# Optimization experiments

Measured on AMD Instinct MI355X. Metric: run time of the kernel, lower is better.

Reference implementation:

```python
import jax, jax.numpy as jnp
import numpy as np
from jax import lax

K = 31      # avg_pool kernel
PAD = 15    # padding (count_include_pad=True -> divide by K*K always)
LAMBDA1 = 1.0
LAMBDA2 = 1.0


def _box_mean(x):
    # 31x31 stride-1 avg pool with zero padding, divisor = K*K (torch default count_include_pad=True)
    s = lax.reduce_window(x, 0.0, lax.add, (1, 1, K, K), (1, 1, 1, 1),
                          [(0, 0), (0, 0), (PAD, PAD), (PAD, PAD)])
    return s / float(K * K)


def setup_inputs() -> dict:
    key = jax.random.key(0)
    k1, k2 = jax.random.split(key)
    pred = jax.random.normal(k1, (64, 1, 512, 512), dtype=jnp.float32)
    mask = jax.random.uniform(k2, (64, 1, 512, 512), dtype=jnp.float32)
    return {"pred": pred, "mask": mask}


def reference(pred, mask):
    weit = 1.0 + 5.0 * jnp.abs(_box_mean(mask) - mask)
    # bce_with_logits, numerically stable: max(x,0) - x*y + log1p(exp(-|x|))
    bce = jnp.maximum(pred, 0.0) - pred * mask + jnp.log1p(jnp.exp(-jnp.abs(pred)))
    # NOTE: original torch code passes reduce='none' (deprecated kwarg, truthy string),
    # which resolves to reduction='mean' -> wbce is a SCALAR; the (weit*.)/weit.sum
    # normalization then cancels exactly. We reproduce that behavior faithfully.
    wbce = jnp.mean(bce)  # scalar, broadcast over (B, C)
    p = jax.nn.sigmoid(pred)
    inter = jnp.sum(p * mask * weit, axis=(2, 3))       # [B, C]
    union = jnp.sum((p + mask) * weit, axis=(2, 3))     # [B, C]
    wiou = 1.0 - (inter + 1.0) / (union - inter + 1.0)  # [B, C]
    return jnp.mean(LAMBDA1 * wbce + LAMBDA2 * wiou)
```

## Files before the change

### kernel.cpp

```cpp
#include <hip/hip_runtime.h>
#include <math.h>

#define BATCH 64
#define HH 512
#define WW 512
#define PAD 15
#define NELEM ((size_t)BATCH * HH * WW)
#define INV_KK (1.0f / 961.0f)

#define TILE_H 32
#define BPI (HH / TILE_H)
#define NBLK (BATCH * BPI)

typedef float f4 __attribute__((ext_vector_type(4)));

__device__ __forceinline__ float wave_reduce(float v) {
    #pragma unroll
    for (int off = 32; off; off >>= 1) v += __shfl_down(v, off, 64);
    return v;
}

__global__ __launch_bounds__(256) void fused_kernel(const float* __restrict__ pred,
                                                    const float* __restrict__ mask,
                                                    double* __restrict__ partials) {
    __shared__ float vrow[4][WW];
    __shared__ float P[4][WW];
    __shared__ float red[3][4];

    const int blk  = blockIdx.x;
    const int b    = blk >> 4;
    const int tile = blk & (BPI - 1);
    const int h0   = tile * TILE_H;
    const int tid  = threadIdx.x;
    const int lane = tid & 63;
    const int wv   = tid >> 6;

    const float* mb = mask + (size_t)b * HH * WW;
    const float* pb = pred + (size_t)b * HH * WW;

    const int c0 = tid, c1 = tid + 256;
    float r0 = 0.f, r1 = 0.f;
    {
        int lo = h0 - PAD; if (lo < 0) lo = 0;
        for (int y = lo; y <= h0 + PAD; ++y) {
            r0 += mb[(size_t)y * WW + c0];
            r1 += mb[(size_t)y * WW + c1];
        }
    }

    float accb = 0.f, acci = 0.f, accu = 0.f;

    for (int it = 0; it < TILE_H / 4; ++it) {
        const int hbase = h0 + it * 4;

        #pragma unroll
        for (int j = 0; j < 4; ++j) {
            const int h = hbase + j;
            vrow[j][c0] = r0;
            vrow[j][c1] = r1;
            const int add = h + PAD + 1;
            const int sub = h - PAD;
            float a0 = 0.f, a1 = 0.f, s0 = 0.f, s1 = 0.f;
            if (add < HH) { a0 = mb[(size_t)add * WW + c0]; a1 = mb[(size_t)add * WW + c1]; }
            if (sub >= 0) { s0 = mb[(size_t)sub * WW + c0]; s1 = mb[(size_t)sub * WW + c1]; }
            r0 += a0 - s0;
            r1 += a1 - s1;
        }
        __syncthreads();

        const int h = hbase + wv;
        const size_t rbase = (size_t)h * WW;

        f4 va = *(const f4*)&vrow[wv][8 * lane];
        f4 vb = *(const f4*)&vrow[wv][8 * lane + 4];
        float p0 = va.x;
        float p1 = p0 + va.y;
        float p2 = p1 + va.z;
        float p3 = p2 + va.w;
        float p4 = p3 + vb.x;
        float p5 = p4 + vb.y;
        float p6 = p5 + vb.z;
        float p7 = p6 + vb.w;
        float lanesum = p7;
        float incl = lanesum;
        #pragma unroll
        for (int off = 1; off < 64; off <<= 1) {
            float n = __shfl_up(incl, off, 64);
            if (lane >= off) incl += n;
        }
        const float excl = incl - lanesum;
        f4 Pa, Pb;
        Pa.x = excl + p0; Pa.y = excl + p1; Pa.z = excl + p2; Pa.w = excl + p3;
        Pb.x = excl + p4; Pb.y = excl + p5; Pb.z = excl + p6; Pb.w = excl + p7;
        *(f4*)&P[wv][8 * lane]     = Pa;
        *(f4*)&P[wv][8 * lane + 4] = Pb;
        __syncthreads();

        #pragma unroll
        for (int k = 0; k < 8; ++k) {
            const int w = lane + 64 * k;
            int hiw = w + PAD; if (hiw > WW - 1) hiw = WW - 1;
            float s = P[wv][hiw];
            if (w >= PAD + 1) s -= P[wv][w - PAD - 1];

            const float m  = mb[rbase + w];
            const float pr = pb[rbase + w];

            const float weit = 1.0f + 5.0f * fabsf(s * INV_KK - m);
            const float e    = __expf(-fabsf(pr));
            const float bce  = fmaxf(pr, 0.f) - pr * m + __logf(1.0f + e);
            const float inv  = __builtin_amdgcn_rcpf(1.0f + e);
            const float p    = (pr >= 0.f) ? inv : e * inv;

            accb += bce;
            acci += p * m * weit;
            accu += (p + m) * weit;
        }
    }

    accb = wave_reduce(accb);
    acci = wave_reduce(acci);
    accu = wave_reduce(accu);
    if (lane == 0) { red[0][wv] = accb; red[1][wv] = acci; red[2][wv] = accu; }
    __syncthreads();
    if (tid == 0) {
        double bt = (double)red[0][0] + red[0][1] + red[0][2] + red[0][3];
        double it = (double)red[1][0] + red[1][1] + red[1][2] + red[1][3];
        double ut = (double)red[2][0] + red[2][1] + red[2][2] + red[2][3];
        partials[(size_t)blk * 3 + 0] = bt;
        partials[(size_t)blk * 3 + 1] = it;
        partials[(size_t)blk * 3 + 2] = ut;
    }
}

__global__ __launch_bounds__(256) void finalize_kernel(const double* __restrict__ partials,
                                                       float* __restrict__ out) {
    __shared__ double redbce[4];
    int tid = threadIdx.x, lane = tid & 63, wv = tid >> 6;

    double bsum = 0.0;
    for (int i = tid; i < NBLK; i += 256) bsum += partials[(size_t)i * 3 + 0];
    #pragma unroll
    for (int off = 32; off; off >>= 1) bsum += __shfl_down(bsum, off, 64);
    if (lane == 0) redbce[wv] = bsum;
    __syncthreads();

    double wiou_term = 0.0;
    if (tid < 64) {
        int bb = tid;
        double it = 0.0, ut = 0.0;
        for (int j = 0; j < BPI; ++j) {
            it += partials[(size_t)(bb * BPI + j) * 3 + 1];
            ut += partials[(size_t)(bb * BPI + j) * 3 + 2];
        }
        wiou_term = 1.0 - (it + 1.0) / (ut - it + 1.0);
    }
    if (wv == 0) {
        #pragma unroll
        for (int off = 32; off; off >>= 1) wiou_term += __shfl_down(wiou_term, off, 64);
    }
    if (tid == 0) {
        double wbce = (redbce[0] + redbce[1] + redbce[2] + redbce[3]) / (double)NELEM;
        out[0] = (float)(wbce + wiou_term * (1.0 / 64.0));
    }
}

#define ACC_DOUBLES 129
__global__ __launch_bounds__(256) void rowpass_nows_kernel(const float* __restrict__ pred,
                                                           const float* __restrict__ mask,
                                                           double* __restrict__ acc) {
    __shared__ float vrow[WW];
    __shared__ float red[3][4];
    int b = blockIdx.x / HH;
    int h = blockIdx.x % HH;
    int lo = h - PAD; if (lo < 0) lo = 0;
    int hi = h + PAD; if (hi > HH - 1) hi = HH - 1;
    float s0 = 0.0f, s1 = 0.0f;
    const float* mb = mask + (size_t)b * HH * WW;
    for (int y = lo; y <= hi; ++y) {
        s0 += mb[(size_t)y * WW + threadIdx.x];
        s1 += mb[(size_t)y * WW + threadIdx.x + 256];
    }
    vrow[threadIdx.x]       = s0;
    vrow[threadIdx.x + 256] = s1;
    __syncthreads();

    size_t base = ((size_t)b * HH + h) * WW;
    float bce_p = 0.0f, inter_p = 0.0f, uni_p = 0.0f;
    for (int w = threadIdx.x; w < WW; w += 256) {
        int wlo = w - PAD; if (wlo < 0) wlo = 0;
        int whi = w + PAD; if (whi > WW - 1) whi = WW - 1;
        float s = 0.0f;
        for (int k = wlo; k <= whi; ++k) s += vrow[k];
        float m  = mask[base + w];
        float pr = pred[base + w];
        float weit = 1.0f + 5.0f * fabsf(s * INV_KK - m);
        float e   = expf(-fabsf(pr));
        float bce = fmaxf(pr, 0.0f) - pr * m + log1pf(e);
        float inv = 1.0f / (1.0f + e);
        float p   = (pr >= 0.0f) ? inv : e * inv;
        bce_p += bce; inter_p += p * m * weit; uni_p += (p + m) * weit;
    }
    int lane = threadIdx.x & 63, wvv = threadIdx.x >> 6;
    bce_p = wave_reduce(bce_p); inter_p = wave_reduce(inter_p); uni_p = wave_reduce(uni_p);
    if (lane == 0) { red[0][wvv] = bce_p; red[1][wvv] = inter_p; red[2][wvv] = uni_p; }
    __syncthreads();
    if (threadIdx.x == 0) {
        atomicAdd(&acc[0], (double)(red[0][0] + red[0][1] + red[0][2] + red[0][3]));
        atomicAdd(&acc[1 + b], (double)(red[1][0] + red[1][1] + red[1][2] + red[1][3]));
        atomicAdd(&acc[65 + b], (double)(red[2][0] + red[2][1] + red[2][2] + red[2][3]));
    }
}

__global__ void finalize_atomic_kernel(const double* __restrict__ acc, float* __restrict__ out) {
    int b = threadIdx.x;
    double inter = acc[1 + b];
    double uni   = acc[65 + b];
    double wiou = 1.0 - (inter + 1.0) / (uni - inter + 1.0);
    #pragma unroll
    for (int off = 32; off; off >>= 1) wiou += __shfl_down(wiou, off, 64);
    if (b == 0) {
        double wbce = acc[0] / (double)NELEM;
        out[0] = (float)(wbce + wiou * (1.0 / 64.0));
    }
}

extern "C" void kernel_launch(void* const* d_in, const int* in_sizes, int n_in,
                              void* d_out, int out_size, void* d_ws, size_t ws_size,
                              hipStream_t stream) {
    const float* pred = (const float*)d_in[0];
    const float* mask = (const float*)d_in[1];
    float* out = (float*)d_out;

    const size_t part_bytes = (size_t)NBLK * 3 * sizeof(double);

    if (ws_size >= part_bytes) {
        double* partials = (double*)d_ws;
        fused_kernel<<<NBLK, 256, 0, stream>>>(pred, mask, partials);
        finalize_kernel<<<1, 256, 0, stream>>>(partials, out);
    } else {
        double* acc = (double*)d_ws;
        hipMemsetAsync(acc, 0, ACC_DOUBLES * sizeof(double), stream);
        rowpass_nows_kernel<<<BATCH * HH, 256, 0, stream>>>(pred, mask, acc);
        finalize_atomic_kernel<<<1, 64, 0, stream>>>(acc, out);
    }
}
```

Baseline: 55.77 us.

## Per-wave row strips with register-resident column sums and shuffle-based horizontal box

Each wave now owns an independent strip of 8 rows and 8 contiguous columns per lane, keeping the vertical running sums in registers and loaded as float4. The horizontal 31-wide window is computed from a wave prefix scan plus lane shuffles, so shared-memory staging and the per-row block barriers go away. Blocks are also remapped so each XCD handles contiguous images, which is meant to improve L2 locality. The cost is more redundant vertical-window initialisation per wave (31 rows for every 8 rows of output) and more shuffle instructions.

```diff
diff --git a/kernel.cpp b/kernel.cpp
--- a/kernel.cpp
+++ b/kernel.cpp
@@ -9,8 +9,10 @@
 #define INV_KK (1.0f / 961.0f)
 
 #define TILE_H 32
+#define RPW 8
 #define BPI (HH / TILE_H)
 #define NBLK (BATCH * BPI)
+#define NXCD 8
 
 typedef float f4 __attribute__((ext_vector_type(4)));
 
@@ -20,101 +22,130 @@
     return v;
 }
 
-__global__ __launch_bounds__(256) void fused_kernel(const float* __restrict__ pred,
-                                                    const float* __restrict__ mask,
-                                                    double* __restrict__ partials) {
-    __shared__ float vrow[4][WW];
-    __shared__ float P[4][WW];
+__global__ __launch_bounds__(256, 4) void fused_kernel(const float* __restrict__ pred,
+                                                       const float* __restrict__ mask,
+                                                       double* __restrict__ partials) {
     __shared__ float red[3][4];
 
-    const int blk  = blockIdx.x;
-    const int b    = blk >> 4;
-    const int tile = blk & (BPI - 1);
-    const int h0   = tile * TILE_H;
+    const int f    = blockIdx.x;
+    const int xcd  = f & (NXCD - 1);
+    const int slot = f >> 3;
+    const int img  = xcd * 8 + (slot >> 4);
+    const int tile = slot & (BPI - 1);
+
     const int tid  = threadIdx.x;
     const int lane = tid & 63;
     const int wv   = tid >> 6;
-
-    const float* mb = mask + (size_t)b * HH * WW;
-    const float* pb = pred + (size_t)b * HH * WW;
-
-    const int c0 = tid, c1 = tid + 256;
-    float r0 = 0.f, r1 = 0.f;
+    const int h0   = tile * TILE_H + wv * RPW;
+    const int c    = lane * 8;
+
+    const float* mb = mask + (size_t)img * HH * WW;
+    const float* pb = pred + (size_t)img * HH * WW;
+
+    float r0 = 0.f, r1 = 0.f, r2 = 0.f, r3 = 0.f, r4 = 0.f, r5 = 0.f, r6 = 0.f, r7 = 0.f;
     {
         int lo = h0 - PAD; if (lo < 0) lo = 0;
-        for (int y = lo; y <= h0 + PAD; ++y) {
-            r0 += mb[(size_t)y * WW + c0];
-            r1 += mb[(size_t)y * WW + c1];
+        int hi = h0 + PAD; if (hi > HH - 1) hi = HH - 1;
+        for (int y = lo; y <= hi; ++y) {
+            f4 m0 = *(const f4*)&mb[(size_t)y * WW + c];
+            f4 m1 = *(const f4*)&mb[(size_t)y * WW + c + 4];
+            r0 += m0.x; r1 += m0.y; r2 += m0.z; r3 += m0.w;
+            r4 += m1.x; r5 += m1.y; r6 += m1.z; r7 += m1.w;
         }
     }
 
     float accb = 0.f, acci = 0.f, accu = 0.f;
 
-    for (int it = 0; it < TILE_H / 4; ++it) {
-        const int hbase = h0 + it * 4;
-
-        #pragma unroll
-        for (int j = 0; j < 4; ++j) {
-            const int h = hbase + j;
-            vrow[j][c0] = r0;
-            vrow[j][c1] = r1;
-            const int add = h + PAD + 1;
-            const int sub = h - PAD;
-            float a0 = 0.f, a1 = 0.f, s0 = 0.f, s1 = 0.f;
-            if (add < HH) { a0 = mb[(size_t)add * WW + c0]; a1 = mb[(size_t)add * WW + c1]; }
-            if (sub >= 0) { s0 = mb[(size_t)sub * WW + c0]; s1 = mb[(size_t)sub * WW + c1]; }
-            r0 += a0 - s0;
-            r1 += a1 - s1;
-        }
-        __syncthreads();
-
-        const int h = hbase + wv;
-        const size_t rbase = (size_t)h * WW;
-
-        f4 va = *(const f4*)&vrow[wv][8 * lane];
-        f4 vb = *(const f4*)&vrow[wv][8 * lane + 4];
-        float p0 = va.x;
-        float p1 = p0 + va.y;
-        float p2 = p1 + va.z;
-        float p3 = p2 + va.w;
-        float p4 = p3 + vb.x;
-        float p5 = p4 + vb.y;
-        float p6 = p5 + vb.z;
-        float p7 = p6 + vb.w;
-        float lanesum = p7;
-        float incl = lanesum;
+    #pragma unroll
+    for (int j = 0; j < RPW; ++j) {
+        const int h = h0 + j;
+        const size_t rb = (size_t)h * WW;
+
+        const float p0 = r0;
+        const float p1 = p0 + r1;
+        const float p2 = p1 + r2;
+        const float p3 = p2 + r3;
+        const float p4 = p3 + r4;
+        const float p5 = p4 + r5;
+        const float p6 = p5 + r6;
+        const float p7 = p6 + r7;
+
+        float incl = p7;
         #pragma unroll
         for (int off = 1; off < 64; off <<= 1) {
             float n = __shfl_up(incl, off, 64);
             if (lane >= off) incl += n;
         }
-        const float excl = incl - lanesum;
-        f4 Pa, Pb;
-        Pa.x = excl + p0; Pa.y = excl + p1; Pa.z = excl + p2; Pa.w = excl + p3;
-        Pb.x = excl + p4; Pb.y = excl + p5; Pb.z = excl + p6; Pb.w = excl + p7;
-        *(f4*)&P[wv][8 * lane]     = Pa;
-        *(f4*)&P[wv][8 * lane + 4] = Pb;
-        __syncthreads();
+        const float excl = incl - p7;
+
+        const float P0 = excl + p0, P1 = excl + p1, P2 = excl + p2, P3 = excl + p3;
+        const float P4 = excl + p4, P5 = excl + p5, P6 = excl + p6, P7 = excl + p7;
+
+        const float top = __shfl(P7, 63, 64);
+        const float hi0 = __shfl_down(P7, 1, 64);
+        const float q0 = __shfl_down(P0, 2, 64);
+        const float q1 = __shfl_down(P1, 2, 64);
+        const float q2 = __shfl_down(P2, 2, 64);
+        const float q3 = __shfl_down(P3, 2, 64);
+        const float q4 = __shfl_down(P4, 2, 64);
+        const float q5 = __shfl_down(P5, 2, 64);
+        const float q6 = __shfl_down(P6, 2, 64);
+        const float l0 = __shfl_up(P0, 2, 64);
+        const float l1 = __shfl_up(P1, 2, 64);
+        const float l2 = __shfl_up(P2, 2, 64);
+        const float l3 = __shfl_up(P3, 2, 64);
+        const float l4 = __shfl_up(P4, 2, 64);
+        const float l5 = __shfl_up(P5, 2, 64);
+        const float l6 = __shfl_up(P6, 2, 64);
+        const float l7 = __shfl_up(P7, 2, 64);
+        const bool okHi1 = (lane <= 62);
+        const bool okHi2 = (lane <= 61);
+        const bool hasLo = (lane >= 2);
+
+        float S[8];
+        S[0] = (okHi1 ? hi0 : top) - (hasLo ? l0 : 0.f);
+        S[1] = (okHi2 ? q0  : top) - (hasLo ? l1 : 0.f);
+        S[2] = (okHi2 ? q1  : top) - (hasLo ? l2 : 0.f);
+        S[3] = (okHi2 ? q2  : top) - (hasLo ? l3 : 0.f);
+        S[4] = (okHi2 ? q3  : top) - (hasLo ? l4 : 0.f);
+        S[5] = (okHi2 ? q4  : top) - (hasLo ? l5 : 0.f);
+        S[6] = (okHi2 ? q5  : top) - (hasLo ? l6 : 0.f);
+        S[7] = (okHi2 ? q6  : top) - (hasLo ? l7 : 0.f);
+
+        const f4 mc0 = *(const f4*)&mb[rb + c];
+        const f4 mc1 = *(const f4*)&mb[rb + c + 4];
+        const f4 pc0 = *(const f4*)&pb[rb + c];
+        const f4 pc1 = *(const f4*)&pb[rb + c + 4];
+        const float mm[8] = {mc0.x, mc0.y, mc0.z, mc0.w, mc1.x, mc1.y, mc1.z, mc1.w};
+        const float pp[8] = {pc0.x, pc0.y, pc0.z, pc0.w, pc1.x, pc1.y, pc1.z, pc1.w};
 
         #pragma unroll
         for (int k = 0; k < 8; ++k) {
-            const int w = lane + 64 * k;
-            int hiw = w + PAD; if (hiw > WW - 1) hiw = WW - 1;
-            float s = P[wv][hiw];
-            if (w >= PAD + 1) s -= P[wv][w - PAD - 1];
-
-            const float m  = mb[rbase + w];
-            const float pr = pb[rbase + w];
-
-            const float weit = 1.0f + 5.0f * fabsf(s * INV_KK - m);
+            const float m  = mm[k];
+            const float pr = pp[k];
+            const float weit = 1.0f + 5.0f * fabsf(S[k] * INV_KK - m);
             const float e    = __expf(-fabsf(pr));
             const float bce  = fmaxf(pr, 0.f) - pr * m + __logf(1.0f + e);
             const float inv  = __builtin_amdgcn_rcpf(1.0f + e);
             const float p    = (pr >= 0.f) ? inv : e * inv;
-
             accb += bce;
             acci += p * m * weit;
             accu += (p + m) * weit;
+        }
+
+        const int add = h + PAD + 1;
+        const int sub = h - PAD;
+        if (add < HH) {
+            f4 a0 = *(const f4*)&mb[(size_t)add * WW + c];
+            f4 a1 = *(const f4*)&mb[(size_t)add * WW + c + 4];
+            r0 += a0.x; r1 += a0.y; r2 += a0.z; r3 += a0.w;
+            r4 += a1.x; r5 += a1.y; r6 += a1.z; r7 += a1.w;
+        }
+        if (sub >= 0) {
+            f4 s0 = *(const f4*)&mb[(size_t)sub * WW + c];
+            f4 s1 = *(const f4*)&mb[(size_t)sub * WW + c + 4];
+            r0 -= s0.x; r1 -= s0.y; r2 -= s0.z; r3 -= s0.w;
+            r4 -= s1.x; r5 -= s1.y; r6 -= s1.z; r7 -= s1.w;
         }
     }
 
@@ -127,9 +158,10 @@
         double bt = (double)red[0][0] + red[0][1] + red[0][2] + red[0][3];
         double it = (double)red[1][0] + red[1][1] + red[1][2] + red[1][3];
         double ut = (double)red[2][0] + red[2][1] + red[2][2] + red[2][3];
-        partials[(size_t)blk * 3 + 0] = bt;
-        partials[(size_t)blk * 3 + 1] = it;
-        partials[(size_t)blk * 3 + 2] = ut;
+        const size_t pidx = (size_t)img * BPI + tile;
+        partials[pidx * 3 + 0] = bt;
+        partials[pidx * 3 + 1] = it;
+        partials[pidx * 3 + 2] = ut;
     }
 }
 
```

Result: slower. 137.5 us (+146.5%).

## Halve row tile, remap blocks per XCD, and trim a barrier

Applied to the files above, without the earlier changes.

Halves the rows per block so twice as many blocks run, and remaps block IDs so each XCD processes whole images contiguously for L2 locality of overlapping halo rows. It also drops the barrier after the per-wave prefix-sum write, since each wave reads only its own row, and moves a barrier to the end of each iteration to protect shared buffer reuse. The cost is more redundant initial column-sum reads per block.

```diff
diff --git a/kernel.cpp b/kernel.cpp
--- a/kernel.cpp
+++ b/kernel.cpp
@@ -8,9 +8,10 @@
 #define NELEM ((size_t)BATCH * HH * WW)
 #define INV_KK (1.0f / 961.0f)
 
-#define TILE_H 32
+#define TILE_H 16
 #define BPI (HH / TILE_H)
 #define NBLK (BATCH * BPI)
+#define NXCD 8
 
 typedef float f4 __attribute__((ext_vector_type(4)));
 
@@ -27,29 +28,35 @@
     __shared__ float P[4][WW];
     __shared__ float red[3][4];
 
-    const int blk  = blockIdx.x;
-    const int b    = blk >> 4;
-    const int tile = blk & (BPI - 1);
-    const int h0   = tile * TILE_H;
+    const int f    = blockIdx.x;
+    const int xcd  = f & (NXCD - 1);
+    const int slot = f >> 3;
+    const int img  = xcd * 8 + (slot >> 5);
+    const int tile = slot & (BPI - 1);
+
     const int tid  = threadIdx.x;
     const int lane = tid & 63;
     const int wv   = tid >> 6;
-
-    const float* mb = mask + (size_t)b * HH * WW;
-    const float* pb = pred + (size_t)b * HH * WW;
-
-    const int c0 = tid, c1 = tid + 256;
-    float r0 = 0.f, r1 = 0.f;
+    const int h0   = tile * TILE_H;
+    const int c0   = tid;
+    const int c1   = tid + 256;
+
+    const float* mb = mask + (size_t)img * HH * WW;
+    const float* pb = pred + (size_t)img * HH * WW;
+
+    float r0 = 0.0f, r1 = 0.0f;
     {
         int lo = h0 - PAD; if (lo < 0) lo = 0;
-        for (int y = lo; y <= h0 + PAD; ++y) {
+        int hi = h0 + PAD; if (hi > HH - 1) hi = HH - 1;
+        for (int y = lo; y <= hi; ++y) {
             r0 += mb[(size_t)y * WW + c0];
             r1 += mb[(size_t)y * WW + c1];
         }
     }
 
-    float accb = 0.f, acci = 0.f, accu = 0.f;
-
+    float accb = 0.0f, acci = 0.0f, accu = 0.0f;
+
+    #pragma unroll 1
     for (int it = 0; it < TILE_H / 4; ++it) {
         const int hbase = h0 + it * 4;
 
@@ -60,7 +67,7 @@
             vrow[j][c1] = r1;
             const int add = h + PAD + 1;
             const int sub = h - PAD;
-            float a0 = 0.f, a1 = 0.f, s0 = 0.f, s1 = 0.f;
+            float a0 = 0.0f, a1 = 0.0f, s0 = 0.0f, s1 = 0.0f;
             if (add < HH) { a0 = mb[(size_t)add * WW + c0]; a1 = mb[(size_t)add * WW + c1]; }
             if (sub >= 0) { s0 = mb[(size_t)sub * WW + c0]; s1 = mb[(size_t)sub * WW + c1]; }
             r0 += a0 - s0;
@@ -94,7 +101,6 @@
         Pb.x = excl + p4; Pb.y = excl + p5; Pb.z = excl + p6; Pb.w = excl + p7;
         *(f4*)&P[wv][8 * lane]     = Pa;
         *(f4*)&P[wv][8 * lane + 4] = Pb;
-        __syncthreads();
 
         #pragma unroll
         for (int k = 0; k < 8; ++k) {
@@ -108,14 +114,15 @@
 
             const float weit = 1.0f + 5.0f * fabsf(s * INV_KK - m);
             const float e    = __expf(-fabsf(pr));
-            const float bce  = fmaxf(pr, 0.f) - pr * m + __logf(1.0f + e);
+            const float bce  = fmaxf(pr, 0.0f) - pr * m + __logf(1.0f + e);
             const float inv  = __builtin_amdgcn_rcpf(1.0f + e);
-            const float p    = (pr >= 0.f) ? inv : e * inv;
+            const float p    = (pr >= 0.0f) ? inv : e * inv;
 
             accb += bce;
             acci += p * m * weit;
             accu += (p + m) * weit;
         }
+        __syncthreads();
     }
 
     accb = wave_reduce(accb);
@@ -125,11 +132,12 @@
     __syncthreads();
     if (tid == 0) {
         double bt = (double)red[0][0] + red[0][1] + red[0][2] + red[0][3];
-        double it = (double)red[1][0] + red[1][1] + red[1][2] + red[1][3];
+        double it2 = (double)red[1][0] + red[1][1] + red[1][2] + red[1][3];
         double ut = (double)red[2][0] + red[2][1] + red[2][2] + red[2][3];
-        partials[(size_t)blk * 3 + 0] = bt;
-        partials[(size_t)blk * 3 + 1] = it;
-        partials[(size_t)blk * 3 + 2] = ut;
+        const size_t pidx = (size_t)img * BPI + tile;
+        partials[pidx * 3 + 0] = bt;
+        partials[pidx * 3 + 1] = it2;
+        partials[pidx * 3 + 2] = ut;
     }
 }
 
@@ -169,7 +177,7 @@
 __global__ __launch_bounds__(256) void rowpass_nows_kernel(const float* __restrict__ pred,
                                                            const float* __restrict__ mask,
                                                            double* __restrict__ acc) {
-    __shared__ float vrow[WW];
+    __shared__ float vrow1[WW];
     __shared__ float red[3][4];
     int b = blockIdx.x / HH;
     int h = blockIdx.x % HH;
@@ -181,8 +189,8 @@
         s0 += mb[(size_t)y * WW + threadIdx.x];
         s1 += mb[(size_t)y * WW + threadIdx.x + 256];
     }
-    vrow[threadIdx.x]       = s0;
-    vrow[threadIdx.x + 256] = s1;
+    vrow1[threadIdx.x]       = s0;
+    vrow1[threadIdx.x + 256] = s1;
     __syncthreads();
 
     size_t base = ((size_t)b * HH + h) * WW;
@@ -191,7 +199,7 @@
         int wlo = w - PAD; if (wlo < 0) wlo = 0;
         int whi = w + PAD; if (whi > WW - 1) whi = WW - 1;
         float s = 0.0f;
-        for (int k = wlo; k <= whi; ++k) s += vrow[k];
+        for (int k = wlo; k <= whi; ++k) s += vrow1[k];
         float m  = mask[base + w];
         float pr = pred[base + w];
         float weit = 1.0f + 5.0f * fabsf(s * INV_KK - m);
```

Measured after the change: 61.63 us. 1.11x slower.
